# Performance work log

Hardware: AMD Instinct MI355X
Metric: run time of the kernel (lower is better)

The kernel has to match this reference:

```python
import jax, jax.numpy as jnp
import numpy as np

N_HEADS = 16
DIM = 1024
DPH = DIM // N_HEADS  # 64
NEG_INF = -1e20       # neginf(float32) in the torch source


def setup_inputs() -> dict:
    key0 = jax.random.key(0)
    ks = jax.random.split(key0, 12)
    bs, qlen, nrev, klen = 32, 128, 20, 64
    w = lambda k: jax.random.normal(k, (DIM, DIM), jnp.float32) * 0.02
    return {
        "query": jax.random.normal(ks[0], (bs, qlen, DIM), jnp.float32),
        "key": jax.random.normal(ks[1], (bs, nrev, klen, DIM), jnp.float32),
        "value": jax.random.normal(ks[2], (bs, nrev, klen, DIM), jnp.float32),
        "mask": jax.random.randint(ks[3], (bs, nrev), 0, 2, jnp.int32),
        "mask2": jax.random.randint(ks[4], (bs, nrev, klen), 0, 2, jnp.int32),
        "Wq": w(ks[5]), "bq": jnp.zeros((DIM,), jnp.float32),
        "Wk": w(ks[6]), "bk": jnp.zeros((DIM,), jnp.float32),
        "Wv": w(ks[7]), "bv": jnp.zeros((DIM,), jnp.float32),
        "Wo": w(ks[8]), "bo": jnp.zeros((DIM,), jnp.float32),
        "sa_a": jax.random.normal(ks[9], (DPH, DPH), jnp.float32) * 0.1,
        "sa_b": jax.random.normal(ks[10], (DPH, 1), jnp.float32) * 0.1,
    }


def _forward(query, key, value, mask, mask2,
             Wq, bq, Wk, bk, Wv, bv, Wo, bo, sa_a, sa_b):
    bs, qlen, dim = query.shape
    _, nrev, klen, _ = key.shape
    dph = dim // N_HEADS
    scale = float(dph) ** 0.5

    # linear projections + head split (torch Linear: x @ W.T + b)
    q = (query @ Wq.T + bq).reshape(bs, qlen, N_HEADS, dph)        # [B,Q,H,d]
    k = (key @ Wk.T + bk).reshape(bs, nrev, klen, N_HEADS, dph)    # [B,R,T,H,d]
    v = (value @ Wv.T + bv).reshape(bs, nrev, klen, N_HEADS, dph)  # [B,R,T,H,d]

    # --- token-level attention: per review, q attends over review tokens ---
    scores = jnp.einsum('bqhd,brthd->bhrqt', q, k) / scale          # [B,H,R,Q,T]
    tok_pad = (mask2 == 0)[:, None, :, None, :]                     # [B,1,R,1,T]
    scores = jnp.where(tok_pad, NEG_INF, scores)
    attn_w = jax.nn.softmax(scores, axis=-1)
    att = jnp.einsum('bhrqt,brthd->bhqrd', attn_w, v)               # [B,H,Q,R,d]

    # --- review-level self-attention pooling (SelfAttentionSeq) ---
    # e = tanh(h @ a) @ b ; mask applied only if some reviews have mask==0,
    # and then NONZERO mask positions get -1e30 (faithful to the source).
    e = jnp.tanh(att @ sa_a) @ sa_b                                 # [B,H,Q,R,1]
    e = e[..., 0]                                                   # [B,H,Q,R]
    mf = mask.astype(att.dtype)                                     # [B,R]
    any_zero = (jnp.sum(mask == 0, axis=-1, keepdims=True) > 0).astype(att.dtype)  # [B,1]
    add_mask = (-1e30 * mf) * any_zero                              # [B,R]
    e = e + add_mask[:, None, None, :]
    rev_w = jax.nn.softmax(e, axis=-1)                              # [B,H,Q,R]
    pooled = jnp.einsum('bhqr,bhqrd->bhqd', rev_w, att)             # [B,H,Q,d]

    # merge heads + output projection
    merged = pooled.transpose(0, 2, 1, 3).reshape(bs, qlen, dim)    # [B,Q,D]
    return merged @ Wo.T + bo


def reference(query, key, value, mask, mask2,
              Wq, bq, Wk, bk, Wv, bv, Wo, bo, sa_a, sa_b):
    return _forward(query, key, value, mask, mask2,
                    Wq, bq, Wk, bk, Wv, bv, Wo, bo, sa_a, sa_b)
```

## Files before the change

kernel.cpp:

```cpp
#include <hip/hip_runtime.h>
#include <stdint.h>


typedef __attribute__((ext_vector_type(8))) short bf16x8;
typedef __attribute__((ext_vector_type(4))) float f32x4;
typedef __attribute__((ext_vector_type(4))) unsigned int u32x4;
typedef __attribute__((address_space(1))) const unsigned int as1_t;
typedef __attribute__((address_space(3))) unsigned int as3_t;

#define DEVI static __device__ __forceinline__

DEVI unsigned short f2bf(float f) {
  unsigned int u = __float_as_uint(f);
  u += 0x7fffu + ((u >> 16) & 1u);
  return (unsigned short)(u >> 16);
}
DEVI unsigned int pack2(float a, float b) {
  return (unsigned int)f2bf(a) | ((unsigned int)f2bf(b) << 16);
}
DEVI unsigned int pk2_rhu(float a, float b) {
  unsigned int ua = __float_as_uint(a) + 0x8000u;
  unsigned int ub = __float_as_uint(b) + 0x8000u;
  return (ua >> 16) | (ub & 0xffff0000u);
}

DEVI void gload_lds16(const void* g, void* l) {
  __builtin_amdgcn_global_load_lds((as1_t*)g, (as3_t*)l, 16, 0, 0);
}

DEVI float fast_tanh(float x) {
  float ax = fabsf(x);
  float e = __expf(2.0f * ax);
  float r = __builtin_fmaf(-2.0f, __builtin_amdgcn_rcpf(e + 1.0f), 1.0f);
  return copysignf(r, x);
}

__global__ void cvt_w4(const float* __restrict__ w0, const float* __restrict__ w1,
                       const float* __restrict__ w2, const float* __restrict__ w3,
                       unsigned short* __restrict__ o0, unsigned short* __restrict__ o1,
                       unsigned short* __restrict__ o2, unsigned short* __restrict__ o3) {
  int i = blockIdx.x * 256 + threadIdx.x;
  if (i >= 262144) return;
  f32x4 v;
  uint2 a;
  v = ((const f32x4*)w0)[i]; a.x = pack2(v[0], v[1]); a.y = pack2(v[2], v[3]);
  *(uint2*)(o0 + 4 * (size_t)i) = a;
  v = ((const f32x4*)w1)[i]; a.x = pack2(v[0], v[1]); a.y = pack2(v[2], v[3]);
  *(uint2*)(o1 + 4 * (size_t)i) = a;
  v = ((const f32x4*)w2)[i]; a.x = pack2(v[0], v[1]); a.y = pack2(v[2], v[3]);
  *(uint2*)(o2 + 4 * (size_t)i) = a;
  v = ((const f32x4*)w3)[i]; a.x = pack2(v[0], v[1]); a.y = pack2(v[2], v[3]);
  *(uint2*)(o3 + 4 * (size_t)i) = a;
}

__global__ void cvt_bf16(const float* __restrict__ src,
                         unsigned short* __restrict__ dst, int n8) {
  const int stride = (int)(gridDim.x * blockDim.x);
  for (int i = (int)(blockIdx.x * blockDim.x + threadIdx.x); i < n8; i += stride) {
    f32x4 a = ((const f32x4*)src)[2 * i];
    f32x4 b = ((const f32x4*)src)[2 * i + 1];
    u32x4 o = {pack2(a[0], a[1]), pack2(a[2], a[3]), pack2(b[0], b[1]), pack2(b[2], b[3])};
    ((u32x4*)dst)[i] = o;
  }
}

__global__ void compact_rv(const int* __restrict__ mask, int* __restrict__ out) {
  const int lane = (int)threadIdx.x;
  __shared__ int azs[32];
  if (lane < 32) {
    int z = 0;
#pragma unroll
    for (int r = 0; r < 20; ++r) z |= (mask[lane * 20 + r] == 0) ? 1 : 0;
    azs[lane] = z;
  }
  __syncthreads();
  int base = 0;
  int lasts = 0;
  for (int it = 0; it < 10; ++it) {
    const int s = it * 64 + lane;
    const int bb = s / 20;
    const int actv = azs[bb] ? ((mask[s] == 0) ? 1 : 0) : 1;
    unsigned long long bal = __ballot(actv);
    const int off = (int)__popcll(bal & ((1ull << lane) - 1ull));
    if (actv) {
      out[1 + base + off] = s;
      lasts = s;
    }
    base += (int)__popcll(bal);
  }
#pragma unroll
  for (int d = 1; d < 64; d <<= 1) {
    int o = __shfl_xor(lasts, d);
    lasts = lasts > o ? lasts : o;
  }
  if (lane == 0) {
    out[0] = base;
    out[1 + base] = lasts;
  }
}

__global__ void cvt_act(const float* __restrict__ src,
                        unsigned short* __restrict__ dst,
                        const int* __restrict__ cmp) {
  const int cnt = cmp[0];
  const int n = ((cnt + 1) & ~1) * 8192;
  const int stride = (int)(gridDim.x * blockDim.x);
  for (int u = (int)(blockIdx.x * blockDim.x + threadIdx.x); u < n; u += stride) {
    const int s = u >> 13;
    const int e = u & 8191;
    const size_t so = (size_t)cmp[1 + s] * 65536 + (size_t)e * 8;
    f32x4 a = *(const f32x4*)(src + so);
    f32x4 b = *(const f32x4*)(src + so + 4);
    u32x4 o = {pack2(a[0], a[1]), pack2(a[2], a[3]),
               pack2(b[0], b[1]), pack2(b[2], b[3])};
    *(u32x4*)(dst + (size_t)u * 8) = o;
  }
}

template <int OUT_MODE, int ADT, int SC, int CMP>
__global__ __launch_bounds__(256, 4) void gemm_bt(
    const void* __restrict__ Ain, const unsigned short* __restrict__ W,
    const float* __restrict__ bias, void* __restrict__ Cout, int N, int K, int nnt,
    const int* __restrict__ cmp) {
  __shared__ __align__(16) char smem[32768];
  char* Asb = smem;
  char* Bsb = smem + 16384;
  const int tid = (int)threadIdx.x;
  const int lane = tid & 63, wave = tid >> 6;
  const int lm = lane & 15, l4 = lane >> 4;
  const int nb = (int)gridDim.x;
  const int bx = (int)blockIdx.x;
  const int wr = wave >> 1, wc = wave & 1;

  int mt, nt, cs0, cs1;
  if (CMP) {
    const int cnt = cmp[0];
    const int tiles = (cnt + 1) >> 1;
    if (bx >= tiles * 8) return;
    const int lg = (bx & 7) * tiles + (bx >> 3);
    mt = lg / nnt;
    nt = lg % nnt;
    cs0 = cmp[1 + 2 * mt];
    cs1 = cmp[2 + 2 * mt];
  } else {
    const int lg = (bx & 7) * (nb >> 3) + (bx >> 3);
    mt = lg / nnt;
    nt = lg % nnt;
    cs0 = 2 * mt;
    cs1 = 2 * mt + 1;
  }

  f32x4 zero4 = {0.f, 0.f, 0.f, 0.f};
  f32x4 acc[4][4];
#pragma unroll
  for (int i = 0; i < 4; ++i)
#pragma unroll
    for (int j = 0; j < 4; ++j) acc[i][j] = zero4;

  const int srow = tid >> 2, sblk = tid & 3;
  const int scb = sblk ^ ((srow >> 1) & 3);
  const unsigned short* wpg = W + (size_t)(nt * 128 + srow) * K + scb * 8;
  const int kx = (lm >> 1) & 3;

  const unsigned short* apg =
      (const unsigned short*)Ain + (size_t)(mt * 128 + srow) * K + scb * 8;
  const int NT = K >> 5;
#pragma unroll
  for (int t0 = 0; t0 < 2; ++t0) {
    const int kt = t0 * 32;
    gload_lds16(apg + kt, Asb + t0 * 8192 + tid * 16);
    gload_lds16(apg + (size_t)64 * K + kt, Asb + t0 * 8192 + 4096 + tid * 16);
    gload_lds16(wpg + kt, Bsb + t0 * 8192 + tid * 16);
    gload_lds16(wpg + (size_t)64 * K + kt, Bsb + t0 * 8192 + 4096 + tid * 16);
  }
  int cur = 0;
  for (int t = 0; t < NT; ++t) {
    if (t + 1 < NT)
      asm volatile("s_waitcnt vmcnt(4)" ::: "memory");
    else
      asm volatile("s_waitcnt vmcnt(0)" ::: "memory");
    asm volatile("s_barrier" ::: "memory");
    bf16x8 af[4], bfr[4];
#pragma unroll
    for (int i = 0; i < 4; ++i)
      af[i] = *(const bf16x8*)(Asb + cur * 8192 + (wr * 64 + i * 16 + lm) * 64 +
                               ((l4 ^ kx) * 16));
#pragma unroll
    for (int j = 0; j < 4; ++j)
      bfr[j] = *(const bf16x8*)(Bsb + cur * 8192 + (wc * 64 + j * 16 + lm) * 64 +
                                ((l4 ^ kx) * 16));
#pragma unroll
    for (int i = 0; i < 4; ++i)
#pragma unroll
      for (int j = 0; j < 4; ++j)
        acc[i][j] = __builtin_amdgcn_mfma_f32_16x16x32_bf16(af[i], bfr[j], acc[i][j], 0, 0, 0);
    asm volatile("s_barrier" ::: "memory");
    if (t + 2 < NT) {
      const int kt = (t + 2) * 32;
      gload_lds16(apg + kt, Asb + cur * 8192 + tid * 16);
      gload_lds16(apg + (size_t)64 * K + kt, Asb + cur * 8192 + 4096 + tid * 16);
      gload_lds16(wpg + kt, Bsb + cur * 8192 + tid * 16);
      gload_lds16(wpg + (size_t)64 * K + kt, Bsb + cur * 8192 + 4096 + tid * 16);
    }
    cur ^= 1;
  }

  const int c0o = nt * 128 + wc * 64 + lm;
  float bb[4];
#pragma unroll
  for (int j = 0; j < 4; ++j) bb[j] = bias[c0o + j * 16];
  const int mslot = wr ? cs1 : cs0;

  if (OUT_MODE < 2) {
#pragma unroll
    for (int i = 0; i < 4; ++i)
#pragma unroll
      for (int j = 0; j < 4; ++j)
#pragma unroll
        for (int p = 0; p < 4; ++p) {
          size_t grow = (size_t)mslot * 64 + (l4 * 4 + i * 16 + p);
          size_t idx = grow * N + (size_t)(c0o + j * 16);
          float v = acc[i][j][p] + bb[j];
          if (SC) v *= 0.125f;
          if (OUT_MODE == 1)
            ((unsigned short*)Cout)[idx] = f2bf(v);
          else
            ((float*)Cout)[idx] = v;
        }
  } else {
    const int hh = (nt * 128 + wc * 64) / 64;
    unsigned short* vt = (unsigned short*)Cout;
    const size_t base = ((size_t)mslot * 16 + hh) * 4096;
#pragma unroll
    for (int j = 0; j < 4; ++j) {
      const int d = lm + j * 16;
#pragma unroll
      for (int i = 0; i < 4; ++i) {
        uint2 wv;
        wv.x = pack2(acc[i][j][0] + bb[j], acc[i][j][1] + bb[j]);
        wv.y = pack2(acc[i][j][2] + bb[j], acc[i][j][3] + bb[j]);
        *(uint2*)(vt + base + (size_t)d * 64 + i * 16 + l4 * 4) = wv;
      }
    }
  }
}

__global__ __launch_bounds__(512, 4) void attn2(
    const unsigned short* __restrict__ qb, const unsigned short* __restrict__ kb,
    const unsigned short* __restrict__ vtg, const int* __restrict__ mask,
    const int* __restrict__ mask2, const float* __restrict__ sa_a,
    const float* __restrict__ sa_b, unsigned short* __restrict__ merged) {
  const int h = (int)blockIdx.x;
  const int b = (int)blockIdx.y;
  const int tid = (int)threadIdx.x;
  const int lane = tid & 63, wave = tid >> 6;
  const int lm = lane & 15, l4 = lane >> 4;
  const int sw = (lm & 7) << 4;

  __shared__ unsigned short kv_s[2][2][64 * 64];
  __shared__ unsigned short pa_s[8 * 16 * 64];

  char* kvb0 = (char*)kv_s;
  char* qreg = (char*)kv_s + 16384;
  char* satb = (char*)pa_s;

  unsigned am = 0u;
#pragma unroll
  for (int rr = 0; rr < 20; ++rr)
    am |= (mask[b * 20 + rr] == 0) ? (1u << rr) : 0u;
  const unsigned act = am ? am : 0xFFFFFu;

#pragma unroll
  for (int s = 0; s < 2; ++s) {
    int idx = s * 512 + tid, row = idx >> 3, blk = idx & 7;
    int cb = blk ^ (row & 7);
    gload_lds16(qb + (size_t)(b * 128 + row) * 1024 + h * 64 + cb * 8, qreg + idx * 16);
  }
#pragma unroll
  for (int s = 0; s < 8; ++s) {
    int idx = s * 512 + tid, jj = idx & 63, d = idx >> 6;
    *(unsigned short*)(satb + jj * 128 + ((d * 2) ^ ((jj & 7) << 4))) =
        f2bf(sa_a[d * 64 + jj]);
  }
  const int srow = tid >> 3, sblk = tid & 7;
  const int scb = sblk ^ (srow & 7);
  int r = (int)__builtin_ctz(act);
  unsigned rem = act & (act - 1u);
  gload_lds16(kb + ((size_t)(b * 20 + r) * 64 + srow) * 1024 + h * 64 + scb * 8,
              kvb0 + tid * 16);
  gload_lds16(vtg + ((size_t)(b * 20 + r) * 16 + h) * 4096 + srow * 64 + scb * 8,
              kvb0 + 8192 + tid * 16);

  f32x4 sbv[4];
#pragma unroll
  for (int i = 0; i < 4; ++i) sbv[i] = *(const f32x4*)(sa_b + i * 16 + l4 * 4);

  __syncthreads();

  const char* qrp = qreg + (wave * 16 + lm) * 128;
  bf16x8 qf[2];
  qf[0] = *(const bf16x8*)(qrp + ((l4 * 16) ^ sw));
  qf[1] = *(const bf16x8*)(qrp + ((64 + l4 * 16) ^ sw));
  bf16x8 sfr[2][4];
#pragma unroll
  for (int kk = 0; kk < 2; ++kk)
#pragma unroll
    for (int i = 0; i < 4; ++i)
      sfr[kk][i] = *(const bf16x8*)(satb + (i * 16 + lm) * 128 +
                                    ((kk * 64 + l4 * 16) ^ sw));
  asm volatile("s_waitcnt lgkmcnt(0)" ::: "memory");
  __syncthreads();

  char* pw = (char*)pa_s + wave * 2048 + lm * 128;

  f32x4 zero4 = {0.f, 0.f, 0.f, 0.f};
  f32x4 Pacc[4];
#pragma unroll
  for (int i = 0; i < 4; ++i) Pacc[i] = zero4;
  float m_run = -3.0e38f, s_run = 0.0f;

  int it = 0;
  for (;;) {
    const int pb = it & 1;
    if (it) __syncthreads();
    const int nr = rem ? (int)__builtin_ctz(rem) : -1;
    if (nr >= 0) {
      const int nbuf = pb ^ 1;
      gload_lds16(kb + ((size_t)(b * 20 + nr) * 64 + srow) * 1024 + h * 64 + scb * 8,
                  kvb0 + nbuf * 16384 + tid * 16);
      gload_lds16(vtg + ((size_t)(b * 20 + nr) * 16 + h) * 4096 + srow * 64 + scb * 8,
                  kvb0 + nbuf * 16384 + 8192 + tid * 16);
    }
    const char* kbse = kvb0 + pb * 16384;
    const char* vbse = kvb0 + pb * 16384 + 8192;

    f32x4 sc[4];
#pragma unroll
    for (int i = 0; i < 4; ++i) sc[i] = zero4;
    __builtin_amdgcn_s_setprio(1);
#pragma unroll
    for (int kk = 0; kk < 2; ++kk) {
      bf16x8 kf[4];
#pragma unroll
      for (int i = 0; i < 4; ++i)
        kf[i] = *(const bf16x8*)(kbse + (i * 16 + lm) * 128 + ((kk * 64 + l4 * 16) ^ sw));
#pragma unroll
      for (int i = 0; i < 4; ++i)
        sc[i] = __builtin_amdgcn_mfma_f32_16x16x32_bf16(kf[i], qf[kk], sc[i], 0, 0, 0);
    }
    __builtin_amdgcn_s_setprio(0);

    const int mbase = (b * 20 + r) * 64;
#pragma unroll
    for (int i = 0; i < 4; ++i) {
      int4 m2 = *(const int4*)(mask2 + mbase + i * 16 + l4 * 4);
      sc[i][0] = (m2.x == 0) ? -1e20f : sc[i][0];
      sc[i][1] = (m2.y == 0) ? -1e20f : sc[i][1];
      sc[i][2] = (m2.z == 0) ? -1e20f : sc[i][2];
      sc[i][3] = (m2.w == 0) ? -1e20f : sc[i][3];
    }
    float mx = sc[0][0];
#pragma unroll
    for (int i = 0; i < 4; ++i)
#pragma unroll
      for (int p = 0; p < 4; ++p) mx = fmaxf(mx, sc[i][p]);
    mx = fmaxf(mx, __shfl_xor(mx, 16));
    mx = fmaxf(mx, __shfl_xor(mx, 32));
    float sum = 0.f;
#pragma unroll
    for (int i = 0; i < 4; ++i)
#pragma unroll
      for (int p = 0; p < 4; ++p) {
        float e = __expf(sc[i][p] - mx);
        sc[i][p] = e;
        sum += e;
      }
    sum += __shfl_xor(sum, 16);
    sum += __shfl_xor(sum, 32);
    const float pinv = __builtin_amdgcn_rcpf(sum);

#pragma unroll
    for (int i = 0; i < 4; ++i) {
      uint2 wv;
      wv.x = pk2_rhu(sc[i][0] * pinv, sc[i][1] * pinv);
      wv.y = pk2_rhu(sc[i][2] * pinv, sc[i][3] * pinv);
      *(uint2*)(pw + ((i * 32 + l4 * 8) ^ sw)) = wv;
    }

    f32x4 av[4];
#pragma unroll
    for (int i = 0; i < 4; ++i) av[i] = zero4;
    __builtin_amdgcn_s_setprio(1);
#pragma unroll
    for (int kk = 0; kk < 2; ++kk) {
      bf16x8 pf = *(const bf16x8*)(pw + ((kk * 64 + l4 * 16) ^ sw));
      bf16x8 vf[4];
#pragma unroll
      for (int i = 0; i < 4; ++i)
        vf[i] = *(const bf16x8*)(vbse + (i * 16 + lm) * 128 + ((kk * 64 + l4 * 16) ^ sw));
#pragma unroll
      for (int i = 0; i < 4; ++i)
        av[i] = __builtin_amdgcn_mfma_f32_16x16x32_bf16(vf[i], pf, av[i], 0, 0, 0);
    }
    __builtin_amdgcn_s_setprio(0);

#pragma unroll
    for (int i = 0; i < 4; ++i) {
      uint2 wv;
      wv.x = pk2_rhu(av[i][0], av[i][1]);
      wv.y = pk2_rhu(av[i][2], av[i][3]);
      *(uint2*)(pw + ((i * 32 + l4 * 8) ^ sw)) = wv;
    }

    f32x4 ep[4];
#pragma unroll
    for (int i = 0; i < 4; ++i) ep[i] = zero4;
    __builtin_amdgcn_s_setprio(1);
#pragma unroll
    for (int kk = 0; kk < 2; ++kk) {
      bf16x8 afr = *(const bf16x8*)(pw + ((kk * 64 + l4 * 16) ^ sw));
#pragma unroll
      for (int i = 0; i < 4; ++i)
        ep[i] = __builtin_amdgcn_mfma_f32_16x16x32_bf16(sfr[kk][i], afr, ep[i], 0, 0, 0);
    }
    __builtin_amdgcn_s_setprio(0);
    float a = 0.f;
#pragma unroll
    for (int i = 0; i < 4; ++i)
#pragma unroll
      for (int p = 0; p < 4; ++p) a += fast_tanh(ep[i][p]) * sbv[i][p];
    a += __shfl_xor(a, 16);
    a += __shfl_xor(a, 32);

    const float e_r = a;
    const float mnew = fmaxf(m_run, e_r);
    const float scl = __expf(m_run - mnew);
    const float w = __expf(e_r - mnew);
    s_run = s_run * scl + w;
#pragma unroll
    for (int i = 0; i < 4; ++i)
#pragma unroll
      for (int p = 0; p < 4; ++p) Pacc[i][p] = Pacc[i][p] * scl + w * av[i][p];
    m_run = mnew;

    if (nr < 0) break;
    r = nr;
    rem &= rem - 1u;
    ++it;
  }

  const float inv_s = __builtin_amdgcn_rcpf(s_run);
  unsigned short* mrow = merged + (size_t)(b * 128 + wave * 16 + lm) * 1024 + h * 64;
#pragma unroll
  for (int i = 0; i < 4; ++i) {
    uint2 o;
    o.x = pk2_rhu(Pacc[i][0] * inv_s, Pacc[i][1] * inv_s);
    o.y = pk2_rhu(Pacc[i][2] * inv_s, Pacc[i][3] * inv_s);
    *(uint2*)(mrow + i * 16 + l4 * 4) = o;
  }
}

extern "C" void kernel_launch(void* const* d_in, const int* in_sizes, int n_in,
                              void* d_out, int out_size, void* d_ws, size_t ws_size,
                              hipStream_t stream) {
  (void)in_sizes; (void)n_in; (void)out_size; (void)ws_size;
  const float* query = (const float*)d_in[0];
  const float* key   = (const float*)d_in[1];
  const float* value = (const float*)d_in[2];
  const int*   mask  = (const int*)d_in[3];
  const int*   mask2 = (const int*)d_in[4];
  const float* Wq = (const float*)d_in[5];
  const float* bq = (const float*)d_in[6];
  const float* Wk = (const float*)d_in[7];
  const float* bk = (const float*)d_in[8];
  const float* Wv = (const float*)d_in[9];
  const float* bv = (const float*)d_in[10];
  const float* Wo = (const float*)d_in[11];
  const float* bo = (const float*)d_in[12];
  const float* sa_a = (const float*)d_in[13];
  const float* sa_b = (const float*)d_in[14];

  char* ws = (char*)d_ws;
  size_t off = 0;
  auto carve = [&](size_t bytes) -> char* {
    char* p = ws + off;
    off += (bytes + 255) & ~(size_t)255;
    return p;
  };
  unsigned short* wq_b = (unsigned short*)carve((size_t)1024 * 1024 * 2);
  unsigned short* wk_b = (unsigned short*)carve((size_t)1024 * 1024 * 2);
  unsigned short* wv_b = (unsigned short*)carve((size_t)1024 * 1024 * 2);
  unsigned short* wo_b = (unsigned short*)carve((size_t)1024 * 1024 * 2);
  unsigned short* q_b  = (unsigned short*)carve((size_t)4096 * 1024 * 2);
  unsigned short* k_b  = (unsigned short*)carve((size_t)40960 * 1024 * 2);
  unsigned short* vt_g = (unsigned short*)carve((size_t)40960 * 1024 * 2);
  unsigned short* mrg  = (unsigned short*)carve((size_t)4096 * 1024 * 2);
  int* cmp = (int*)carve(4096);
  unsigned short* act = (unsigned short*)carve((size_t)40960 * 1024 * 2);

  cvt_w4<<<1024, 256, 0, stream>>>(Wq, Wk, Wv, Wo, wq_b, wk_b, wv_b, wo_b);
  compact_rv<<<1, 64, 0, stream>>>(mask, cmp);

  cvt_bf16<<<1024, 256, 0, stream>>>(query, act, 4096 * 1024 / 8);
  gemm_bt<1, 1, 1, 0><<<dim3(32 * 8), 256, 0, stream>>>(act, wq_b, bq, q_b, 1024, 1024, 8, cmp);

  cvt_act<<<2048, 256, 0, stream>>>(key, act, cmp);
  gemm_bt<1, 1, 0, 1><<<dim3(320 * 8), 256, 0, stream>>>(act, wk_b, bk, k_b, 1024, 1024, 8, cmp);

  cvt_act<<<2048, 256, 0, stream>>>(value, act, cmp);
  gemm_bt<2, 1, 0, 1><<<dim3(320 * 8), 256, 0, stream>>>(act, wv_b, bv, vt_g, 1024, 1024, 8, cmp);

  attn2<<<dim3(16, 32), 512, 0, stream>>>(q_b, k_b, vt_g, mask, mask2, sa_a, sa_b, mrg);

  gemm_bt<0, 1, 0, 0><<<dim3(32 * 8), 256, 0, stream>>>(mrg, wo_b, bo, d_out, 1024, 1024, 8, cmp);
}
```

Measured before the change: 266.8 us.

## Fuse prep kernels, use hardware bf16 pack, prefetch mask2 before MFMA

Merges the weight conversion, query conversion and review-compaction kernels into one launch, cutting two kernel launches and their serialization gaps. Replaces the manual round-half-up bf16 packing in the attention kernel with the native v_cvt_pk_bf16_f32 instruction, which uses round-to-nearest-even and so changes rounding slightly. It also hoists the mask2 loads ahead of the QK MFMAs so their latency overlaps compute.

```diff
diff --git a/kernel.cpp b/kernel.cpp
--- a/kernel.cpp
+++ b/kernel.cpp
@@ -18,10 +18,10 @@
 DEVI unsigned int pack2(float a, float b) {
   return (unsigned int)f2bf(a) | ((unsigned int)f2bf(b) << 16);
 }
-DEVI unsigned int pk2_rhu(float a, float b) {
-  unsigned int ua = __float_as_uint(a) + 0x8000u;
-  unsigned int ub = __float_as_uint(b) + 0x8000u;
-  return (ua >> 16) | (ub & 0xffff0000u);
+DEVI unsigned int cvtpk(float a, float b) {
+  unsigned int r;
+  asm("v_cvt_pk_bf16_f32 %0, %1, %2" : "=v"(r) : "v"(a), "v"(b));
+  return r;
 }
 
 DEVI void gload_lds16(const void* g, void* l) {
@@ -35,67 +35,73 @@
   return copysignf(r, x);
 }
 
-__global__ void cvt_w4(const float* __restrict__ w0, const float* __restrict__ w1,
-                       const float* __restrict__ w2, const float* __restrict__ w3,
-                       unsigned short* __restrict__ o0, unsigned short* __restrict__ o1,
-                       unsigned short* __restrict__ o2, unsigned short* __restrict__ o3) {
-  int i = blockIdx.x * 256 + threadIdx.x;
-  if (i >= 262144) return;
-  f32x4 v;
-  uint2 a;
-  v = ((const f32x4*)w0)[i]; a.x = pack2(v[0], v[1]); a.y = pack2(v[2], v[3]);
-  *(uint2*)(o0 + 4 * (size_t)i) = a;
-  v = ((const f32x4*)w1)[i]; a.x = pack2(v[0], v[1]); a.y = pack2(v[2], v[3]);
-  *(uint2*)(o1 + 4 * (size_t)i) = a;
-  v = ((const f32x4*)w2)[i]; a.x = pack2(v[0], v[1]); a.y = pack2(v[2], v[3]);
-  *(uint2*)(o2 + 4 * (size_t)i) = a;
-  v = ((const f32x4*)w3)[i]; a.x = pack2(v[0], v[1]); a.y = pack2(v[2], v[3]);
-  *(uint2*)(o3 + 4 * (size_t)i) = a;
-}
-
-__global__ void cvt_bf16(const float* __restrict__ src,
-                         unsigned short* __restrict__ dst, int n8) {
-  const int stride = (int)(gridDim.x * blockDim.x);
-  for (int i = (int)(blockIdx.x * blockDim.x + threadIdx.x); i < n8; i += stride) {
-    f32x4 a = ((const f32x4*)src)[2 * i];
-    f32x4 b = ((const f32x4*)src)[2 * i + 1];
-    u32x4 o = {pack2(a[0], a[1]), pack2(a[2], a[3]), pack2(b[0], b[1]), pack2(b[2], b[3])};
-    ((u32x4*)dst)[i] = o;
-  }
-}
-
-__global__ void compact_rv(const int* __restrict__ mask, int* __restrict__ out) {
-  const int lane = (int)threadIdx.x;
-  __shared__ int azs[32];
-  if (lane < 32) {
-    int z = 0;
-#pragma unroll
-    for (int r = 0; r < 20; ++r) z |= (mask[lane * 20 + r] == 0) ? 1 : 0;
-    azs[lane] = z;
-  }
-  __syncthreads();
-  int base = 0;
-  int lasts = 0;
-  for (int it = 0; it < 10; ++it) {
-    const int s = it * 64 + lane;
-    const int bb = s / 20;
-    const int actv = azs[bb] ? ((mask[s] == 0) ? 1 : 0) : 1;
-    unsigned long long bal = __ballot(actv);
-    const int off = (int)__popcll(bal & ((1ull << lane) - 1ull));
-    if (actv) {
-      out[1 + base + off] = s;
-      lasts = s;
-    }
-    base += (int)__popcll(bal);
-  }
-#pragma unroll
-  for (int d = 1; d < 64; d <<= 1) {
-    int o = __shfl_xor(lasts, d);
-    lasts = lasts > o ? lasts : o;
-  }
-  if (lane == 0) {
-    out[0] = base;
-    out[1 + base] = lasts;
+__global__ __launch_bounds__(256) void prep(
+    const float* __restrict__ w0, const float* __restrict__ w1,
+    const float* __restrict__ w2, const float* __restrict__ w3,
+    unsigned short* __restrict__ o0, unsigned short* __restrict__ o1,
+    unsigned short* __restrict__ o2, unsigned short* __restrict__ o3,
+    const float* __restrict__ qsrc, unsigned short* __restrict__ qdst,
+    const int* __restrict__ mask, int* __restrict__ cmp) {
+  const int bx = (int)blockIdx.x;
+  const int tid = (int)threadIdx.x;
+  if (bx < 1024) {
+    const int i = bx * 256 + tid;
+    f32x4 v;
+    uint2 a;
+    v = ((const f32x4*)w0)[i]; a.x = pack2(v[0], v[1]); a.y = pack2(v[2], v[3]);
+    *(uint2*)(o0 + 4 * (size_t)i) = a;
+    v = ((const f32x4*)w1)[i]; a.x = pack2(v[0], v[1]); a.y = pack2(v[2], v[3]);
+    *(uint2*)(o1 + 4 * (size_t)i) = a;
+    v = ((const f32x4*)w2)[i]; a.x = pack2(v[0], v[1]); a.y = pack2(v[2], v[3]);
+    *(uint2*)(o2 + 4 * (size_t)i) = a;
+    v = ((const f32x4*)w3)[i]; a.x = pack2(v[0], v[1]); a.y = pack2(v[2], v[3]);
+    *(uint2*)(o3 + 4 * (size_t)i) = a;
+  } else if (bx < 2048) {
+    const int i = (bx - 1024) * 256 + tid;
+#pragma unroll
+    for (int h = 0; h < 2; ++h) {
+      const int u = i + h * 262144;
+      f32x4 a = ((const f32x4*)qsrc)[2 * u];
+      f32x4 b = ((const f32x4*)qsrc)[2 * u + 1];
+      u32x4 o = {pack2(a[0], a[1]), pack2(a[2], a[3]),
+                 pack2(b[0], b[1]), pack2(b[2], b[3])};
+      ((u32x4*)qdst)[u] = o;
+    }
+  } else {
+    __shared__ int azs[32];
+    if (tid < 32) {
+      int z = 0;
+#pragma unroll
+      for (int r = 0; r < 20; ++r) z |= (mask[tid * 20 + r] == 0) ? 1 : 0;
+      azs[tid] = z;
+    }
+    __syncthreads();
+    if (tid < 64) {
+      const int lane = tid;
+      int base = 0;
+      int lasts = 0;
+      for (int it = 0; it < 10; ++it) {
+        const int s = it * 64 + lane;
+        const int bb = s / 20;
+        const int actv = azs[bb] ? ((mask[s] == 0) ? 1 : 0) : 1;
+        unsigned long long bal = __ballot(actv);
+        const int off = (int)__popcll(bal & ((1ull << lane) - 1ull));
+        if (actv) {
+          cmp[1 + base + off] = s;
+          lasts = s;
+        }
+        base += (int)__popcll(bal);
+      }
+#pragma unroll
+      for (int d = 1; d < 64; d <<= 1) {
+        int o = __shfl_xor(lasts, d);
+        lasts = lasts > o ? lasts : o;
+      }
+      if (lane == 0) {
+        cmp[0] = base;
+        cmp[1 + base] = lasts;
+      }
+    }
   }
 }
 
@@ -334,6 +340,12 @@
     const char* kbse = kvb0 + pb * 16384;
     const char* vbse = kvb0 + pb * 16384 + 8192;
 
+    const int mbase = (b * 20 + r) * 64;
+    int4 m2v[4];
+#pragma unroll
+    for (int i = 0; i < 4; ++i)
+      m2v[i] = *(const int4*)(mask2 + mbase + i * 16 + l4 * 4);
+
     f32x4 sc[4];
 #pragma unroll
     for (int i = 0; i < 4; ++i) sc[i] = zero4;
@@ -350,14 +362,12 @@
     }
     __builtin_amdgcn_s_setprio(0);
 
-    const int mbase = (b * 20 + r) * 64;
 #pragma unroll
     for (int i = 0; i < 4; ++i) {
-      int4 m2 = *(const int4*)(mask2 + mbase + i * 16 + l4 * 4);
-      sc[i][0] = (m2.x == 0) ? -1e20f : sc[i][0];
-      sc[i][1] = (m2.y == 0) ? -1e20f : sc[i][1];
-      sc[i][2] = (m2.z == 0) ? -1e20f : sc[i][2];
-      sc[i][3] = (m2.w == 0) ? -1e20f : sc[i][3];
+      sc[i][0] = (m2v[i].x == 0) ? -1e20f : sc[i][0];
+      sc[i][1] = (m2v[i].y == 0) ? -1e20f : sc[i][1];
+      sc[i][2] = (m2v[i].z == 0) ? -1e20f : sc[i][2];
+      sc[i][3] = (m2v[i].w == 0) ? -1e20f : sc[i][3];
     }
     float mx = sc[0][0];
 #pragma unroll
@@ -382,8 +392,8 @@
 #pragma unroll
     for (int i = 0; i < 4; ++i) {
       uint2 wv;
-      wv.x = pk2_rhu(sc[i][0] * pinv, sc[i][1] * pinv);
-      wv.y = pk2_rhu(sc[i][2] * pinv, sc[i][3] * pinv);
+      wv.x = cvtpk(sc[i][0] * pinv, sc[i][1] * pinv);
+      wv.y = cvtpk(sc[i][2] * pinv, sc[i][3] * pinv);
       *(uint2*)(pw + ((i * 32 + l4 * 8) ^ sw)) = wv;
     }
 
@@ -407,8 +417,8 @@
 #pragma unroll
     for (int i = 0; i < 4; ++i) {
       uint2 wv;
-      wv.x = pk2_rhu(av[i][0], av[i][1]);
-      wv.y = pk2_rhu(av[i][2], av[i][3]);
+      wv.x = cvtpk(av[i][0], av[i][1]);
+      wv.y = cvtpk(av[i][2], av[i][3]);
       *(uint2*)(pw + ((i * 32 + l4 * 8) ^ sw)) = wv;
     }
 
@@ -454,8 +464,8 @@
 #pragma unroll
   for (int i = 0; i < 4; ++i) {
     uint2 o;
-    o.x = pk2_rhu(Pacc[i][0] * inv_s, Pacc[i][1] * inv_s);
-    o.y = pk2_rhu(Pacc[i][2] * inv_s, Pacc[i][3] * inv_s);
+    o.x = cvtpk(Pacc[i][0] * inv_s, Pacc[i][1] * inv_s);
+    o.y = cvtpk(Pacc[i][2] * inv_s, Pacc[i][3] * inv_s);
     *(uint2*)(mrow + i * 16 + l4 * 4) = o;
   }
 }
@@ -498,10 +508,9 @@
   int* cmp = (int*)carve(4096);
   unsigned short* act = (unsigned short*)carve((size_t)40960 * 1024 * 2);
 
-  cvt_w4<<<1024, 256, 0, stream>>>(Wq, Wk, Wv, Wo, wq_b, wk_b, wv_b, wo_b);
-  compact_rv<<<1, 64, 0, stream>>>(mask, cmp);
-
-  cvt_bf16<<<1024, 256, 0, stream>>>(query, act, 4096 * 1024 / 8);
+  prep<<<2049, 256, 0, stream>>>(Wq, Wk, Wv, Wo, wq_b, wk_b, wv_b, wo_b,
+                                 query, act, mask, cmp);
+
   gemm_bt<1, 1, 1, 0><<<dim3(32 * 8), 256, 0, stream>>>(act, wq_b, bq, q_b, 1024, 1024, 8, cmp);
 
   cvt_act<<<2048, 256, 0, stream>>>(key, act, cmp);
```

Measured after the change: 259.0 us. 1.03x faster.
